# Performance work log

Hardware: AMD Instinct MI355X
Metric: run time of the kernel (lower is better)

Reference implementation:

```python
import jax, jax.numpy as jnp
import numpy as np

B, T, D = 4096, 200, 64
H1, H2 = 80, 40
CONST_MIN = -4294967295.0


def setup_inputs() -> dict:
    key = jax.random.key(0)
    ks = jax.random.split(key, 10)
    scale1 = 1.0 / np.sqrt(4 * D)
    scale2 = 1.0 / np.sqrt(H1)
    scalef = 1.0 / np.sqrt(H2)
    return {
        "q": jax.random.normal(ks[0], (B, D), dtype=jnp.float32),
        "k": jax.random.normal(ks[1], (B, T, D), dtype=jnp.float32),
        "v": jax.random.normal(ks[2], (B, T, D), dtype=jnp.float32),
        "mask": jax.random.randint(ks[3], (B, T), 0, 2, dtype=jnp.int32),
        "W1": jax.random.normal(ks[4], (4 * D, H1), dtype=jnp.float32) * scale1,
        "b1": jnp.zeros((H1,), dtype=jnp.float32),
        "W2": jax.random.normal(ks[5], (H1, H2), dtype=jnp.float32) * scale2,
        "b2": jnp.zeros((H2,), dtype=jnp.float32),
        "Wf": jax.random.normal(ks[6], (H2, 1), dtype=jnp.float32) * scalef,
        "bf": jnp.zeros((1,), dtype=jnp.float32),
    }


def reference(q, k, v, mask, W1, b1, W2, b2, Wf, bf):
    # q: [B, D] -> broadcast to [B, T, D] (tile + reshape in the original)
    qt = jnp.broadcast_to(q[:, None, :], k.shape)
    # concat [q, k, q-k, q*k] -> [B, T, 4D]
    info = jnp.concatenate([qt, k, qt - k, qt * k], axis=-1)
    # small MLP: 4D -> H1 -> H2 -> 1, relu activations on hidden layers
    info = jax.nn.relu(jnp.einsum('btf,fh->bth', info, W1) + b1)
    info = jax.nn.relu(jnp.einsum('bth,hg->btg', info, W2) + b2)
    logits = (jnp.einsum('btg,go->bto', info, Wf) + bf)[..., 0]  # [B, T]
    # masked softmax over T
    logits = jnp.where(mask == 0, jnp.float32(CONST_MIN), logits)
    attn = jax.nn.softmax(logits, axis=-1)  # [B, T]
    # weighted sum over v -> [B, D]
    return jnp.einsum('bt,btd->bd', attn, v)
```

## Files before the change

### kernel.cpp

```cpp
#include <hip/hip_runtime.h>
#include <cstddef>
#include <cmath>

#define NB  4096
#define TT  200
#define DD  64
#define NH1 80
#define NH2 40

typedef _Float16 half8 __attribute__((ext_vector_type(8)));
typedef float    f32x4 __attribute__((ext_vector_type(4)));

static const size_t OFF_QH = 0;
static const size_t OFF_F1 = (size_t)NB * NH1 * 4;
static const size_t OFF_F2 = OFF_F1 + (size_t)5 * 4 * 64 * 8 * 2;

__global__ void prep_weights(const float* __restrict__ W1, const float* __restrict__ W2,
                             _Float16* __restrict__ wF1, _Float16* __restrict__ wF2)
{
    const int tid = blockIdx.x * blockDim.x + threadIdx.x;
    const int stride = blockDim.x * gridDim.x;
    for (int i = tid; i < 5 * 4 * 64 * 8; i += stride) {
        const int j = i & 7, l = (i >> 3) & 63, s = (i >> 9) & 3, n = i >> 11;
        const int h  = n * 16 + (l & 15);
        const int kk = s * 32 + (l >> 4) * 8 + j;
        const float w = (kk < 64) ? (W1[(64 + kk) * NH1 + h] - W1[(128 + kk) * NH1 + h])
                                  :  W1[(128 + kk) * NH1 + h];
        wF1[i] = (_Float16)w;
    }
    for (int i = tid; i < 3 * 3 * 64 * 8; i += stride) {
        const int j = i & 7, l = (i >> 3) & 63;
        const int s = (i >> 9) % 3, n = i / 1536;
        const int kk = s * 32 + (l >> 4) * 8 + j;
        const int n2 = n * 16 + (l & 15);
        const float w = (kk < NH1 && n2 < NH2) ? W2[kk * NH2 + n2] : 0.f;
        wF2[i] = (_Float16)w;
    }
}

__global__ void prep_qh(const float* __restrict__ q, const float* __restrict__ W1,
                        const float* __restrict__ b1, float* __restrict__ wQh)
{
    const int idx = blockIdx.x * blockDim.x + threadIdx.x;
    if (idx >= NB * NH1) return;
    const int b = idx / NH1;
    const int h = idx - b * NH1;
    const float* qb = q + (size_t)b * DD;
    float acc = b1[h];
#pragma unroll 8
    for (int d = 0; d < DD; ++d)
        acc += qb[d] * (W1[d * NH1 + h] + W1[(128 + d) * NH1 + h]);
    wQh[idx] = acc;
}

__global__ __launch_bounds__(256, 2)
void attn_main(const float* __restrict__ q, const float* __restrict__ k,
               const float* __restrict__ v, const int* __restrict__ mask,
               const float* __restrict__ Wf, const float* __restrict__ b2g,
               const float* __restrict__ bf,
               const float* __restrict__ wQh, const _Float16* __restrict__ wF1,
               const _Float16* __restrict__ wF2, float* __restrict__ out)
{
    __shared__ __align__(16) _Float16 sWF1[5 * 4 * 64 * 8];
    __shared__ __align__(16) char sH1[4 * 3072];
    __shared__ float sBias[4][208];

    const int tid  = threadIdx.x;
    const int wid  = tid >> 6;
    const int lane = tid & 63;
    const int lr   = lane & 15;
    const int lg   = lane >> 4;
    const int b    = blockIdx.x * 4 + wid;
    const float bfv = bf[0];

    {
        f32x4* dst = (f32x4*)sWF1;
        const f32x4* src = (const f32x4*)wF1;
        for (int i = tid; i < 1280; i += 256) dst[i] = src[i];
    }

    for (int i = lane; i < 208; i += 64) {
        float bv;
        if (i < TT) bv = mask[(size_t)b * TT + i] ? 3.0e38f : -4294967295.0f;
        else        bv = -INFINITY;
        sBias[wid][i] = bv;
    }

    half8 w2f[9];
#pragma unroll
    for (int i = 0; i < 9; ++i) w2f[i] = ((const half8*)wF2)[i * 64 + lane];

    float qhr[5];
#pragma unroll
    for (int n = 0; n < 5; ++n) qhr[n] = wQh[(size_t)b * NH1 + n * 16 + lr];
    float wfr[3], bbr[3];
#pragma unroll
    for (int n = 0; n < 3; ++n) {
        const int hc = n * 16 + lr;
        wfr[n] = (hc < NH2) ? Wf[hc]  : 0.f;
        bbr[n] = (hc < NH2) ? b2g[hc] : 0.f;
    }

    half8 qh0, qh1;
    {
        const float* qb = q + (size_t)b * DD;
#pragma unroll
        for (int j = 0; j < 8; ++j) qh0[j] = (_Float16)qb[lg * 8 + j];
#pragma unroll
        for (int j = 0; j < 8; ++j) qh1[j] = (_Float16)qb[32 + lg * 8 + j];
    }

    char* myH1 = sH1 + wid * 3072;
    if (lane < 32) {
        const int row = lane >> 1;
        const int slotL = 10 + (lane & 1);
        const f32x4 z4 = {};
        *(f32x4*)(myH1 + row * 192 + ((slotL ^ (row & 3)) << 4)) = z4;
    }

    __syncthreads();

    const half8* sF1v = (const half8*)sWF1;
    const float* vb   = v + (size_t)b * (TT * DD);

    float m = -INFINITY, s = 0.f, acc = 0.f;

    for (int mt = 0; mt < 13; ++mt) {
        const int t = min(mt * 16 + lr, TT - 1);
        const float* krow = k + ((size_t)b * TT + t) * DD;
        const f32x4 kv0 = *(const f32x4*)(krow + lg * 8);
        const f32x4 kv1 = *(const f32x4*)(krow + lg * 8 + 4);
        const f32x4 kv2 = *(const f32x4*)(krow + 32 + lg * 8);
        const f32x4 kv3 = *(const f32x4*)(krow + 32 + lg * 8 + 4);

        half8 af[4];
#pragma unroll
        for (int j = 0; j < 4; ++j) {
            af[0][j] = (_Float16)kv0[j];  af[0][j + 4] = (_Float16)kv1[j];
            af[1][j] = (_Float16)kv2[j];  af[1][j + 4] = (_Float16)kv3[j];
        }
        af[2] = qh0 * af[0];
        af[3] = qh1 * af[1];

#pragma unroll
        for (int n = 0; n < 5; ++n) {
            f32x4 a = {};
#pragma unroll
            for (int ss = 0; ss < 4; ++ss)
                a = __builtin_amdgcn_mfma_f32_16x16x32_f16(af[ss], sF1v[(n * 4 + ss) * 64 + lane], a, 0, 0, 0);
            const int slot   = (n * 16 + lr) >> 3;
            const int within = ((n * 16 + lr) & 7) * 2;
#pragma unroll
            for (int j = 0; j < 4; ++j) {
                const int r = lg * 4 + j;
                const float hv = fmaxf(a[j] + qhr[n], 0.f);
                *(_Float16*)(myH1 + r * 192 + ((slot ^ (r & 3)) << 4) + within) = (_Float16)hv;
            }
        }

        half8 a2[3];
#pragma unroll
        for (int ss = 0; ss < 3; ++ss)
            a2[ss] = *(const half8*)(myH1 + lr * 192 + (((ss * 4 + lg) ^ (lr & 3)) << 4));

        float p0 = 0.f, p1 = 0.f, p2 = 0.f, p3 = 0.f;
#pragma unroll
        for (int n = 0; n < 3; ++n) {
            f32x4 c2 = {};
#pragma unroll
            for (int ss = 0; ss < 3; ++ss)
                c2 = __builtin_amdgcn_mfma_f32_16x16x32_f16(a2[ss], w2f[n * 3 + ss], c2, 0, 0, 0);
            p0 += fmaxf(c2[0] + bbr[n], 0.f) * wfr[n];
            p1 += fmaxf(c2[1] + bbr[n], 0.f) * wfr[n];
            p2 += fmaxf(c2[2] + bbr[n], 0.f) * wfr[n];
            p3 += fmaxf(c2[3] + bbr[n], 0.f) * wfr[n];
        }
#pragma unroll
        for (int off = 1; off < 16; off <<= 1) {
            p0 += __shfl_xor(p0, off);
            p1 += __shfl_xor(p1, off);
            p2 += __shfl_xor(p2, off);
            p3 += __shfl_xor(p3, off);
        }

        float l[16];
#pragma unroll
        for (int g = 0; g < 4; ++g) {
            const int src = g << 4;
            l[g * 4 + 0] = __shfl(p0, src);
            l[g * 4 + 1] = __shfl(p1, src);
            l[g * 4 + 2] = __shfl(p2, src);
            l[g * 4 + 3] = __shfl(p3, src);
        }

        float lmax = -INFINITY;
#pragma unroll
        for (int j = 0; j < 16; ++j) {
            l[j] = fminf(l[j] + bfv, sBias[wid][mt * 16 + j]);
            lmax = fmaxf(lmax, l[j]);
        }
        const float mnew  = fmaxf(m, lmax);
        const float scale = __expf(m - mnew);
        acc *= scale;
        s   *= scale;
        m    = mnew;
#pragma unroll
        for (int j = 0; j < 16; ++j) {
            const float w = __expf(l[j] - mnew);
            s += w;
            const int tj = min(mt * 16 + j, TT - 1);
            acc = fmaf(w, vb[tj * DD + lane], acc);
        }
    }

    out[(size_t)b * DD + lane] = acc / s;
}

extern "C" void kernel_launch(void* const* d_in, const int* in_sizes, int n_in,
                              void* d_out, int out_size, void* d_ws, size_t ws_size,
                              hipStream_t stream)
{
    const float* q   = (const float*)d_in[0];
    const float* k   = (const float*)d_in[1];
    const float* v   = (const float*)d_in[2];
    const int*  mask = (const int*)  d_in[3];
    const float* W1  = (const float*)d_in[4];
    const float* b1  = (const float*)d_in[5];
    const float* W2  = (const float*)d_in[6];
    const float* b2  = (const float*)d_in[7];
    const float* Wf  = (const float*)d_in[8];
    const float* bf  = (const float*)d_in[9];
    float* out = (float*)d_out;

    char* ws = (char*)d_ws;
    float*    wQh = (float*)   (ws + OFF_QH);
    _Float16* wF1 = (_Float16*)(ws + OFF_F1);
    _Float16* wF2 = (_Float16*)(ws + OFF_F2);

    prep_weights<<<16, 256, 0, stream>>>(W1, W2, wF1, wF2);
    prep_qh<<<(NB * NH1 + 255) / 256, 256, 0, stream>>>(q, W1, b1, wQh);
    attn_main<<<NB / 4, 256, 0, stream>>>(q, k, v, mask, Wf, b2, bf, wQh, wF1, wF2, out);
}
```

Baseline: 102.7 us.

## Prefetch next K tile, vectorize V loads, split online softmax across lane groups

The next 16-row K tile is loaded into registers before the current tile's MFMAs run, so global load latency overlaps compute. The online softmax is split so each 16-lane group keeps its own running max, sum and a 4-wide accumulator over 4 rows of V, using float4 loads instead of 16 scalar loads per lane. The partial states are merged with cross-group shuffles at the end. The qh and b2 biases are folded into the MFMA accumulator initial values, and the logit broadcast shuffles are removed. The cost is more live registers, which at launch bounds (256,2) could cause spills.

```diff
diff --git a/kernel.cpp b/kernel.cpp
--- a/kernel.cpp
+++ b/kernel.cpp
@@ -63,7 +63,7 @@
 {
     __shared__ __align__(16) _Float16 sWF1[5 * 4 * 64 * 8];
     __shared__ __align__(16) char sH1[4 * 3072];
-    __shared__ float sBias[4][208];
+    __shared__ __align__(16) float sBias[4][208];
 
     const int tid  = threadIdx.x;
     const int wid  = tid >> 6;
@@ -71,6 +71,7 @@
     const int lr   = lane & 15;
     const int lg   = lane >> 4;
     const int b    = blockIdx.x * 4 + wid;
+    const int d0   = lr * 4;
     const float bfv = bf[0];
 
     {
@@ -123,57 +124,75 @@
     const half8* sF1v = (const half8*)sWF1;
     const float* vb   = v + (size_t)b * (TT * DD);
 
-    float m = -INFINITY, s = 0.f, acc = 0.f;
+    float m = -INFINITY, s = 0.f;
+    f32x4 acc = {};
+
+    f32x4 kc0, kc1, kc2, kc3;
+    {
+        const float* krow = k + ((size_t)b * TT + lr) * DD;
+        kc0 = *(const f32x4*)(krow + lg * 8);
+        kc1 = *(const f32x4*)(krow + lg * 8 + 4);
+        kc2 = *(const f32x4*)(krow + 32 + lg * 8);
+        kc3 = *(const f32x4*)(krow + 32 + lg * 8 + 4);
+    }
 
     for (int mt = 0; mt < 13; ++mt) {
-        const int t = min(mt * 16 + lr, TT - 1);
-        const float* krow = k + ((size_t)b * TT + t) * DD;
-        const f32x4 kv0 = *(const f32x4*)(krow + lg * 8);
-        const f32x4 kv1 = *(const f32x4*)(krow + lg * 8 + 4);
-        const f32x4 kv2 = *(const f32x4*)(krow + 32 + lg * 8);
-        const f32x4 kv3 = *(const f32x4*)(krow + 32 + lg * 8 + 4);
-
-        half8 af[4];
+        const int tr = mt * 16 + lg * 4;
+        const f32x4 vA = *(const f32x4*)(vb + (size_t)min(tr + 0, TT - 1) * DD + d0);
+        const f32x4 vB = *(const f32x4*)(vb + (size_t)min(tr + 1, TT - 1) * DD + d0);
+        const f32x4 vC = *(const f32x4*)(vb + (size_t)min(tr + 2, TT - 1) * DD + d0);
+        const f32x4 vD = *(const f32x4*)(vb + (size_t)min(tr + 3, TT - 1) * DD + d0);
+
+        half8 af0, af1;
 #pragma unroll
         for (int j = 0; j < 4; ++j) {
-            af[0][j] = (_Float16)kv0[j];  af[0][j + 4] = (_Float16)kv1[j];
-            af[1][j] = (_Float16)kv2[j];  af[1][j + 4] = (_Float16)kv3[j];
-        }
-        af[2] = qh0 * af[0];
-        af[3] = qh1 * af[1];
+            af0[j] = (_Float16)kc0[j];  af0[j + 4] = (_Float16)kc1[j];
+            af1[j] = (_Float16)kc2[j];  af1[j + 4] = (_Float16)kc3[j];
+        }
+        const half8 af2 = qh0 * af0;
+        const half8 af3 = qh1 * af1;
+
+        if (mt < 12) {
+            const int t = min((mt + 1) * 16 + lr, TT - 1);
+            const float* krow = k + ((size_t)b * TT + t) * DD;
+            kc0 = *(const f32x4*)(krow + lg * 8);
+            kc1 = *(const f32x4*)(krow + lg * 8 + 4);
+            kc2 = *(const f32x4*)(krow + 32 + lg * 8);
+            kc3 = *(const f32x4*)(krow + 32 + lg * 8 + 4);
+        }
 
 #pragma unroll
         for (int n = 0; n < 5; ++n) {
-            f32x4 a = {};
-#pragma unroll
-            for (int ss = 0; ss < 4; ++ss)
-                a = __builtin_amdgcn_mfma_f32_16x16x32_f16(af[ss], sF1v[(n * 4 + ss) * 64 + lane], a, 0, 0, 0);
+            f32x4 a = { qhr[n], qhr[n], qhr[n], qhr[n] };
+            a = __builtin_amdgcn_mfma_f32_16x16x32_f16(af0, sF1v[(n * 4 + 0) * 64 + lane], a, 0, 0, 0);
+            a = __builtin_amdgcn_mfma_f32_16x16x32_f16(af1, sF1v[(n * 4 + 1) * 64 + lane], a, 0, 0, 0);
+            a = __builtin_amdgcn_mfma_f32_16x16x32_f16(af2, sF1v[(n * 4 + 2) * 64 + lane], a, 0, 0, 0);
+            a = __builtin_amdgcn_mfma_f32_16x16x32_f16(af3, sF1v[(n * 4 + 3) * 64 + lane], a, 0, 0, 0);
             const int slot   = (n * 16 + lr) >> 3;
             const int within = ((n * 16 + lr) & 7) * 2;
 #pragma unroll
             for (int j = 0; j < 4; ++j) {
                 const int r = lg * 4 + j;
-                const float hv = fmaxf(a[j] + qhr[n], 0.f);
+                const float hv = fmaxf(a[j], 0.f);
                 *(_Float16*)(myH1 + r * 192 + ((slot ^ (r & 3)) << 4) + within) = (_Float16)hv;
             }
         }
 
-        half8 a2[3];
-#pragma unroll
-        for (int ss = 0; ss < 3; ++ss)
-            a2[ss] = *(const half8*)(myH1 + lr * 192 + (((ss * 4 + lg) ^ (lr & 3)) << 4));
+        half8 a2_0 = *(const half8*)(myH1 + lr * 192 + (((0 * 4 + lg) ^ (lr & 3)) << 4));
+        half8 a2_1 = *(const half8*)(myH1 + lr * 192 + (((1 * 4 + lg) ^ (lr & 3)) << 4));
+        half8 a2_2 = *(const half8*)(myH1 + lr * 192 + (((2 * 4 + lg) ^ (lr & 3)) << 4));
 
         float p0 = 0.f, p1 = 0.f, p2 = 0.f, p3 = 0.f;
 #pragma unroll
         for (int n = 0; n < 3; ++n) {
-            f32x4 c2 = {};
-#pragma unroll
-            for (int ss = 0; ss < 3; ++ss)
-                c2 = __builtin_amdgcn_mfma_f32_16x16x32_f16(a2[ss], w2f[n * 3 + ss], c2, 0, 0, 0);
-            p0 += fmaxf(c2[0] + bbr[n], 0.f) * wfr[n];
-            p1 += fmaxf(c2[1] + bbr[n], 0.f) * wfr[n];
-            p2 += fmaxf(c2[2] + bbr[n], 0.f) * wfr[n];
-            p3 += fmaxf(c2[3] + bbr[n], 0.f) * wfr[n];
+            f32x4 c2 = { bbr[n], bbr[n], bbr[n], bbr[n] };
+            c2 = __builtin_amdgcn_mfma_f32_16x16x32_f16(a2_0, w2f[n * 3 + 0], c2, 0, 0, 0);
+            c2 = __builtin_amdgcn_mfma_f32_16x16x32_f16(a2_1, w2f[n * 3 + 1], c2, 0, 0, 0);
+            c2 = __builtin_amdgcn_mfma_f32_16x16x32_f16(a2_2, w2f[n * 3 + 2], c2, 0, 0, 0);
+            p0 = fmaf(fmaxf(c2[0], 0.f), wfr[n], p0);
+            p1 = fmaf(fmaxf(c2[1], 0.f), wfr[n], p1);
+            p2 = fmaf(fmaxf(c2[2], 0.f), wfr[n], p2);
+            p3 = fmaf(fmaxf(c2[3], 0.f), wfr[n], p3);
         }
 #pragma unroll
         for (int off = 1; off < 16; off <<= 1) {
@@ -183,37 +202,45 @@
             p3 += __shfl_xor(p3, off);
         }
 
-        float l[16];
-#pragma unroll
-        for (int g = 0; g < 4; ++g) {
-            const int src = g << 4;
-            l[g * 4 + 0] = __shfl(p0, src);
-            l[g * 4 + 1] = __shfl(p1, src);
-            l[g * 4 + 2] = __shfl(p2, src);
-            l[g * 4 + 3] = __shfl(p3, src);
-        }
-
-        float lmax = -INFINITY;
-#pragma unroll
-        for (int j = 0; j < 16; ++j) {
-            l[j] = fminf(l[j] + bfv, sBias[wid][mt * 16 + j]);
-            lmax = fmaxf(lmax, l[j]);
-        }
-        const float mnew  = fmaxf(m, lmax);
-        const float scale = __expf(m - mnew);
-        acc *= scale;
-        s   *= scale;
-        m    = mnew;
-#pragma unroll
-        for (int j = 0; j < 16; ++j) {
-            const float w = __expf(l[j] - mnew);
-            s += w;
-            const int tj = min(mt * 16 + j, TT - 1);
-            acc = fmaf(w, vb[tj * DD + lane], acc);
-        }
-    }
-
-    out[(size_t)b * DD + lane] = acc / s;
+        const f32x4 bias4 = *(const f32x4*)&sBias[wid][mt * 16 + lg * 4];
+        const float l0 = fminf(p0, bias4[0]) + bfv;
+        const float l1 = fminf(p1, bias4[1]) + bfv;
+        const float l2 = fminf(p2, bias4[2]) + bfv;
+        const float l3 = fminf(p3, bias4[3]) + bfv;
+        const float lmax = fmaxf(fmaxf(l0, l1), fmaxf(l2, l3));
+        const float mnew = fmaxf(m, lmax);
+        const float sc = __expf(m - mnew);
+        const float w0 = __expf(l0 - mnew);
+        const float w1 = __expf(l1 - mnew);
+        const float w2 = __expf(l2 - mnew);
+        const float w3 = __expf(l3 - mnew);
+        s = s * sc + (w0 + w1 + w2 + w3);
+        acc *= sc;
+        acc += vA * w0;
+        acc += vB * w1;
+        acc += vC * w2;
+        acc += vD * w3;
+        m = mnew;
+    }
+
+    float mo = fmaxf(m, __shfl_xor(m, 16));
+    mo = fmaxf(mo, __shfl_xor(mo, 32));
+    const float f = __expf(m - mo);
+    s *= f;
+    acc *= f;
+    s += __shfl_xor(s, 16);
+    s += __shfl_xor(s, 32);
+#pragma unroll
+    for (int e = 0; e < 4; ++e) {
+        float t = acc[e];
+        t += __shfl_xor(t, 16);
+        t += __shfl_xor(t, 32);
+        acc[e] = t;
+    }
+    if (lg == 0) {
+        const f32x4 res = acc / s;
+        *(f32x4*)(out + (size_t)b * DD + d0) = res;
+    }
 }
 
 extern "C" void kernel_launch(void* const* d_in, const int* in_sizes, int n_in,
```

Result: no change. 101.3 us (-1.3%).
